# Optimization experiments

Hardware: AMD Instinct MI355X
Metric: run time of the kernel (lower is better)

Reference implementation:

```python
import jax, jax.numpy as jnp
import numpy as np

B, N, D = 2, 8192, 64          # batch, points, feature dim (dim_in == dim_out)
FILTER_SIZE = 11               # k nearest neighbors in feature space
N_ITER = 5                     # mean-field iterations


def setup_inputs() -> dict:
    key = jax.random.key(0)
    k0, k1, k2, k3 = jax.random.split(key, 4)
    return {
        "logits": jax.random.normal(k0, (B, N), jnp.float32),
        "p": jax.random.normal(k1, (B, D, N), jnp.float32),
        "W1": jax.random.normal(k2, (D, D), jnp.float32) / np.float32(np.sqrt(D)),
        "b1": jnp.zeros((D,), jnp.float32),
        "W2": jax.random.normal(k3, (D, D), jnp.float32) / np.float32(np.sqrt(D)),
        "b2": jnp.zeros((D,), jnp.float32),
    }


def reference(logits, p, W1, b1, W2, b2):
    # crf_encoder: two stacked Linear layers applied to p.permute(0,2,1) -> [B,N,D]
    f = jnp.einsum('bdn,de->bne', p, W1) + b1
    f = jnp.einsum('bne,ef->bnf', f, W2) + b2  # [B,N,D] feature embedding

    # pairwise squared distances in feature space: [B,N,N]
    sq = jnp.sum(f * f, axis=-1)
    d2 = sq[:, :, None] + sq[:, None, :] - 2.0 * jnp.einsum('bnd,bmd->bnm', f, f)

    # filter_size nearest neighbors (includes self) with Gaussian weights exp(-d2)
    neg_d2, idx = jax.lax.top_k(-d2, FILTER_SIZE)   # [B,N,K]
    w = jnp.exp(neg_d2)                             # [B,N,K]

    gather = jax.vmap(lambda qb, ib: qb[ib])        # per-batch gather: [N],[N,K]->[N,K]

    # mean-field iterations (binary CRF: sigmoid marginals, unary = logits)
    u = logits
    for _ in range(N_ITER):
        q = jax.nn.sigmoid(u)                       # current marginals [B,N]
        msg = jnp.sum(w * gather(q, idx), axis=-1)  # filtered message   [B,N]
        u = logits - msg                            # compatibility transform + unary

    return jax.nn.sigmoid(u)  # return_log_proba=False -> probabilities, [B,N]
```

## Files before the change

kernel.cpp:

```cpp
#include <hip/hip_runtime.h>

#define NPTS 8192
#define NTOT 16384
#define KNB 11
#define CAP 16
#define MARG 9.0f
#define MAXM 8192

typedef __attribute__((ext_vector_type(8))) short short8;
typedef __attribute__((ext_vector_type(4))) float f32x4;

__device__ __forceinline__ unsigned short f2bf(float x) {
  union { float f; unsigned u; } v; v.f = x;
  unsigned r = v.u + 0x7FFFu + ((v.u >> 16) & 1u);
  return (unsigned short)(r >> 16);
}

__device__ __forceinline__ float sigm(float x) { return 1.f / (1.f + expf(-x)); }

__global__ __launch_bounds__(256) void k1_encode(
    const float* __restrict__ p,
    const float* __restrict__ W1,
    const float* __restrict__ b1,
    const float* __restrict__ W2,
    const float* __restrict__ b2,
    float* __restrict__ f32f,
    unsigned short* __restrict__ fpre,
    float* __restrict__ sq,
    float* __restrict__ sq32,
    unsigned* __restrict__ cnt,
    int* __restrict__ lctr) {
  __shared__ float sp[64 * 64];
  __shared__ float st[64 * 65];
  __shared__ float sPart[4][64];
  int t = threadIdx.x, lane = t & 63;
  int w = __builtin_amdgcn_readfirstlane(t >> 6);
  int e0 = w * 16;
  int base = blockIdx.x * 64;
  int b = base >> 13, n0 = base & (NPTS - 1);
  const float* pb = p + (size_t)b * 64 * NPTS + n0;

  if (w == 0) cnt[base + lane] = 0u;
  if (base == 0 && t == 0) *lctr = 0;

  int row = t >> 4, chunk = t & 15;
#pragma unroll
  for (int k = 0; k < 4; ++k) {
    int r = k * 16 + row;
    uint4 v = *(const uint4*)(pb + (size_t)r * NPTS + chunk * 4);
    *(uint4*)(sp + r * 64 + chunk * 4) = v;
  }
  __syncthreads();

  float tt[16];
#pragma unroll
  for (int j = 0; j < 16; ++j) tt[j] = b1[e0 + j];
#pragma unroll 8
  for (int d = 0; d < 64; ++d) {
    float pd = sp[d * 64 + lane];
#pragma unroll
    for (int j = 0; j < 16; ++j)
      tt[j] = fmaf(pd, W1[d * 64 + e0 + j], tt[j]);
  }
#pragma unroll
  for (int j = 0; j < 16; ++j) st[lane * 65 + e0 + j] = tt[j];
  __syncthreads();

  float f[16];
#pragma unroll
  for (int j = 0; j < 16; ++j) f[j] = b2[e0 + j];
#pragma unroll 8
  for (int d = 0; d < 64; ++d) {
    float td = st[lane * 65 + d];
#pragma unroll
    for (int j = 0; j < 16; ++j)
      f[j] = fmaf(td, W2[d * 64 + e0 + j], f[j]);
  }

  float s = 0.f;
#pragma unroll
  for (int j = 0; j < 16; ++j) s = fmaf(f[j], f[j], s);
  sPart[w][lane] = s;
  __syncthreads();
  if (w == 0) {
    float s32 = sPart[0][lane] + sPart[1][lane];
    float s64 = s32 + (sPart[2][lane] + sPart[3][lane]);
    sq32[base + lane] = s32;
    sq[base + lane] = s64;
  }

  f32x4* o4 = (f32x4*)(f32f + (size_t)(base + lane) * 64 + e0);
#pragma unroll
  for (int jj = 0; jj < 4; ++jj) {
    f32x4 v; v[0] = f[4 * jj]; v[1] = f[4 * jj + 1]; v[2] = f[4 * jj + 2]; v[3] = f[4 * jj + 3];
    o4[jj] = v;
  }
  if (w < 2) {
    unsigned* ob = (unsigned*)(fpre + (size_t)(base + lane) * 32 + e0);
#pragma unroll
    for (int jj = 0; jj < 8; ++jj) {
      unsigned lo = f2bf(f[2 * jj]);
      unsigned hi = f2bf(f[2 * jj + 1]);
      ob[jj] = lo | (hi << 16);
    }
  }
}

__global__ __launch_bounds__(256) void k2_gram_select(
    const unsigned short* __restrict__ fpre,
    const float* __restrict__ sq32,
    unsigned* __restrict__ cnt,
    unsigned* __restrict__ cand,
    int* __restrict__ lctr,
    int* __restrict__ list) {
  __shared__ uint4 sB[1024];
  int bid = blockIdx.x;
  int b = (bid >= 528) ? 1 : 0;
  int rem = bid - b * 528;
  int band = (int)((sqrtf(8.f * (float)rem + 1.f) - 1.f) * 0.5f);
  if (((band + 1) * (band + 2)) / 2 <= rem) band++;
  else if ((band * (band + 1)) / 2 > rem) band--;
  int seg = rem - (band * (band + 1)) / 2;

  int t = threadIdx.x;
  int lane = t & 63;
  int arow = lane & 15;
  int q = lane >> 4;
  int wave = t >> 6;
  int rowbase = band * 256 + wave * 64;
  int cbase = seg * 256;
  const unsigned short* fb = fpre + (size_t)b * NPTS * 32;
  const float* s32b = sq32 + b * NPTS;

  const uint4* gsrc = (const uint4*)fb + (size_t)seg * 1024;
  uint4 v[4];
#pragma unroll
  for (int k = 0; k < 4; ++k) v[k] = gsrc[t + k * 256];

  short8 afrag[4];
#pragma unroll
  for (int tr = 0; tr < 4; ++tr)
    afrag[tr] = *(const short8*)(fb + (size_t)(rowbase + tr * 16 + arow) * 32 + q * 8);

  f32x4 srq[4], hh[4];
#pragma unroll
  for (int tr = 0; tr < 4; ++tr) {
    srq[tr] = *(const f32x4*)(s32b + rowbase + tr * 16 + (q << 2));
    hh[tr] = 0.5f * srq[tr];
  }
  float thrc[16];
#pragma unroll
  for (int cc = 0; cc < 4; ++cc)
#pragma unroll
    for (int tc = 0; tc < 4; ++tc)
      thrc[cc * 4 + tc] = 0.5f * s32b[cbase + cc * 64 + tc * 16 + arow] - 0.5f * MARG;

#pragma unroll
  for (int k = 0; k < 4; ++k) {
    int c = t + k * 256;
    int r = c >> 2, qq = c & 3;
    sB[r * 4 + (qq ^ (r & 3))] = v[k];
  }
  __syncthreads();

  f32x4 z4 = {0.f, 0.f, 0.f, 0.f};
  unsigned hitmask = 0u;
#pragma unroll
  for (int cc = 0; cc < 4; ++cc)
#pragma unroll
    for (int tc = 0; tc < 4; ++tc) {
      int e = cc * 4 + tc;
      int rl = cc * 64 + tc * 16 + arow;
      short8 bf = *(const short8*)&sB[rl * 4 + (q ^ (rl & 3))];
      f32x4 a0 = __builtin_amdgcn_mfma_f32_16x16x32_bf16(afrag[0], bf, z4, 0, 0, 0);
      f32x4 a1 = __builtin_amdgcn_mfma_f32_16x16x32_bf16(afrag[1], bf, z4, 0, 0, 0);
      f32x4 a2 = __builtin_amdgcn_mfma_f32_16x16x32_bf16(afrag[2], bf, z4, 0, 0, 0);
      f32x4 a3 = __builtin_amdgcn_mfma_f32_16x16x32_bf16(afrag[3], bf, z4, 0, 0, 0);
      float m0 = fmaxf(fmaxf(a0[0] - hh[0][0], a0[1] - hh[0][1]),
                       fmaxf(a0[2] - hh[0][2], a0[3] - hh[0][3]));
      float m1 = fmaxf(fmaxf(a1[0] - hh[1][0], a1[1] - hh[1][1]),
                       fmaxf(a1[2] - hh[1][2], a1[3] - hh[1][3]));
      float m2 = fmaxf(fmaxf(a2[0] - hh[2][0], a2[1] - hh[2][1]),
                       fmaxf(a2[2] - hh[2][2], a2[3] - hh[2][3]));
      float m3 = fmaxf(fmaxf(a3[0] - hh[3][0], a3[1] - hh[3][1]),
                       fmaxf(a3[2] - hh[3][2], a3[3] - hh[3][3]));
      float m = fmaxf(fmaxf(m0, m1), fmaxf(m2, m3));
      if (__ballot(m > thrc[e])) hitmask |= (1u << e);
    }

  if (hitmask) {
#pragma unroll 1
    for (int e = 0; e < 16; ++e) {
      if (!(hitmask & (1u << e))) continue;
      int cc = e >> 2, tc = e & 3;
      int rl = cc * 64 + tc * 16 + arow;
      short8 bf = *(const short8*)&sB[rl * 4 + (q ^ (rl & 3))];
      int colpt = cbase + cc * 64 + tc * 16 + arow;
      float scv = s32b[colpt];
      f32x4 acc[4];
#pragma unroll
      for (int tr = 0; tr < 4; ++tr)
        acc[tr] = __builtin_amdgcn_mfma_f32_16x16x32_bf16(afrag[tr], bf, z4, 0, 0, 0);
#pragma unroll
      for (int tr = 0; tr < 4; ++tr)
#pragma unroll
        for (int rg = 0; rg < 4; ++rg) {
          float d2 = srq[tr][rg] + scv - 2.f * acc[tr][rg];
          if (d2 < MARG) {
            int rowpt = rowbase + tr * 16 + (q << 2) + rg;
            int gr = b * NPTS + rowpt;
            union { float f; unsigned u; } cv; cv.f = d2 + 16.f;
            unsigned kb = cv.u & 0xFFFFE000u;
            unsigned slot = atomicAdd(&cnt[gr], 1u);
            if (slot < CAP) cand[gr * CAP + slot] = kb | (unsigned)colpt;
            if (slot == 1u) {
              int ls = atomicAdd(lctr, 1);
              if (ls < MAXM) list[ls] = gr;
            }
            if (band != seg) {
              int gc = b * NPTS + colpt;
              unsigned slot2 = atomicAdd(&cnt[gc], 1u);
              if (slot2 < CAP) cand[gc * CAP + slot2] = kb | (unsigned)rowpt;
              if (slot2 == 1u) {
                int ls2 = atomicAdd(lctr, 1);
                if (ls2 < MAXM) list[ls2] = gc;
              }
            }
          }
        }
    }
  }
}

__global__ __launch_bounds__(256) void k3_fused(
    const float* __restrict__ f32f, const float* __restrict__ sq,
    const unsigned* __restrict__ cnt, const unsigned* __restrict__ cand,
    float* __restrict__ Wbuf, int* __restrict__ IDXb,
    const float* __restrict__ logits, float* __restrict__ out) {
  int r = blockIdx.x * 256 + threadIdx.x;
  int b = r >> 13;
  unsigned count = cnt[r];
  if (count <= 1u) {
    float lg = logits[r];
    float u = lg;
#pragma unroll
    for (int it = 0; it < 5; ++it) u = lg - sigm(u);
    out[r] = sigm(u);
    return;
  }
  if (count > CAP) count = CAP;

  unsigned k[CAP];
#pragma unroll
  for (int j = 0; j < CAP; ++j)
    k[j] = (j < (int)count) ? cand[r * CAP + j] : 0xFFFFFFFFu;
#pragma unroll
  for (int a = 0; a < CAP - 1; ++a)
#pragma unroll
    for (int c = 0; c < CAP - 1; ++c) {
      unsigned lo = min(k[c], k[c + 1]);
      unsigned hi = max(k[c], k[c + 1]);
      k[c] = lo; k[c + 1] = hi;
    }

  float fr[64];
  const f32x4* fr4 = (const f32x4*)(f32f + (size_t)r * 64);
#pragma unroll
  for (int j = 0; j < 16; ++j) {
    f32x4 v = fr4[j];
    fr[4 * j] = v[0]; fr[4 * j + 1] = v[1]; fr[4 * j + 2] = v[2]; fr[4 * j + 3] = v[3];
  }
  float sqr = sq[r];
  int nsel = (int)count < KNB ? (int)count : KNB;
#pragma unroll
  for (int kk = 0; kk < KNB; ++kk) {
    float w = 0.f;
    int gi = r;
    if (kk < nsel) {
      int col = (int)(k[kk] & 8191u);
      gi = b * NPTS + col;
      const float* fm = f32f + (size_t)gi * 64;
      float dot = 0.f;
#pragma unroll
      for (int d = 0; d < 64; ++d) dot = fmaf(fr[d], fm[d], dot);
      float d2 = sqr + sq[gi] - 2.f * dot;
      w = expf(-d2);
    }
    Wbuf[(size_t)r * KNB + kk] = w;
    IDXb[(size_t)r * KNB + kk] = gi;
  }
}

__global__ __launch_bounds__(1024) void kt_iter(
    const int* __restrict__ lctr, const int* __restrict__ list,
    const float* __restrict__ Wbuf, const int* __restrict__ IDXb,
    const float* __restrict__ logits, float* __restrict__ out) {
  __shared__ float qs[NTOT];
  __shared__ int slist[MAXM];
  __shared__ float su[MAXM];
  int t = threadIdx.x;
  int nm = *lctr; if (nm > MAXM) nm = MAXM;

#pragma unroll 1
  for (int k = t; k < nm; k += 1024) {
    int r = list[k];
    slist[k] = r;
    qs[r] = sigm(logits[r]);
  }
  __syncthreads();

  for (int it = 0; it < 5; ++it) {
#pragma unroll 1
    for (int k = t; k < nm; k += 1024) {
      int r = slist[k];
      float msg = 0.f;
      const float* wp = Wbuf + (size_t)r * KNB;
      const int* ip = IDXb + (size_t)r * KNB;
#pragma unroll
      for (int kk = 0; kk < KNB; ++kk) msg = fmaf(wp[kk], qs[ip[kk]], msg);
      su[k] = logits[r] - msg;
    }
    __syncthreads();
#pragma unroll 1
    for (int k = t; k < nm; k += 1024) qs[slist[k]] = sigm(su[k]);
    __syncthreads();
  }
#pragma unroll 1
  for (int k = t; k < nm; k += 1024) out[slist[k]] = sigm(su[k]);
}

extern "C" void kernel_launch(void* const* d_in, const int* in_sizes, int n_in,
                              void* d_out, int out_size, void* d_ws, size_t ws_size,
                              hipStream_t stream) {
  const float* logits = (const float*)d_in[0];
  const float* p      = (const float*)d_in[1];
  const float* W1     = (const float*)d_in[2];
  const float* b1     = (const float*)d_in[3];
  const float* W2     = (const float*)d_in[4];
  const float* b2     = (const float*)d_in[5];
  float* out = (float*)d_out;

  char* ws = (char*)d_ws;
  float* f32f = (float*)ws;
  unsigned short* fpre = (unsigned short*)(f32f + (size_t)NTOT * 64);
  float* sq = (float*)(fpre + (size_t)NTOT * 32);
  float* sq32 = sq + NTOT;
  unsigned* cnt = (unsigned*)(sq32 + NTOT);
  unsigned* cand = cnt + NTOT;
  float* Wbuf = (float*)(cand + (size_t)NTOT * CAP);
  int* IDX = (int*)(Wbuf + (size_t)NTOT * KNB);
  int* lctr = IDX + (size_t)NTOT * KNB;
  int* list = lctr + 1;

  k1_encode<<<256, 256, 0, stream>>>(p, W1, b1, W2, b2, f32f, fpre, sq, sq32, cnt, lctr);
  k2_gram_select<<<1056, 256, 0, stream>>>(fpre, sq32, cnt, cand, lctr, list);
  k3_fused<<<64, 256, 0, stream>>>(f32f, sq, cnt, cand, Wbuf, IDX, logits, out);
  kt_iter<<<1, 1024, 0, stream>>>(lctr, list, Wbuf, IDX, logits, out);
}
```

Measured before the change: 111.8 us.

## Fold row norm into MFMA accumulator and fuse neighbor weighting with iteration kernel

In the gram/select kernel, the row half-norm is passed as the negated MFMA accumulator init, so the per-element subtraction in the screening loop goes away. The k3 and kt_iter kernels are merged into one 65-block launch. Blocks 0-63 handle isolated points, and the last block (256 threads) does sorting, distance/weight computation and all mean-field iterations for the listed points. This removes one launch, but the per-candidate weight work moves from 64 parallel blocks onto a single 256-thread block, which may serialize it.

```diff
diff --git a/kernel.cpp b/kernel.cpp
--- a/kernel.cpp
+++ b/kernel.cpp
@@ -142,11 +142,11 @@
   for (int tr = 0; tr < 4; ++tr)
     afrag[tr] = *(const short8*)(fb + (size_t)(rowbase + tr * 16 + arow) * 32 + q * 8);
 
-  f32x4 srq[4], hh[4];
+  f32x4 srq[4], nh[4];
 #pragma unroll
   for (int tr = 0; tr < 4; ++tr) {
     srq[tr] = *(const f32x4*)(s32b + rowbase + tr * 16 + (q << 2));
-    hh[tr] = 0.5f * srq[tr];
+    nh[tr] = -0.5f * srq[tr];
   }
   float thrc[16];
 #pragma unroll
@@ -163,7 +163,6 @@
   }
   __syncthreads();
 
-  f32x4 z4 = {0.f, 0.f, 0.f, 0.f};
   unsigned hitmask = 0u;
 #pragma unroll
   for (int cc = 0; cc < 4; ++cc)
@@ -172,18 +171,14 @@
       int e = cc * 4 + tc;
       int rl = cc * 64 + tc * 16 + arow;
       short8 bf = *(const short8*)&sB[rl * 4 + (q ^ (rl & 3))];
-      f32x4 a0 = __builtin_amdgcn_mfma_f32_16x16x32_bf16(afrag[0], bf, z4, 0, 0, 0);
-      f32x4 a1 = __builtin_amdgcn_mfma_f32_16x16x32_bf16(afrag[1], bf, z4, 0, 0, 0);
-      f32x4 a2 = __builtin_amdgcn_mfma_f32_16x16x32_bf16(afrag[2], bf, z4, 0, 0, 0);
-      f32x4 a3 = __builtin_amdgcn_mfma_f32_16x16x32_bf16(afrag[3], bf, z4, 0, 0, 0);
-      float m0 = fmaxf(fmaxf(a0[0] - hh[0][0], a0[1] - hh[0][1]),
-                       fmaxf(a0[2] - hh[0][2], a0[3] - hh[0][3]));
-      float m1 = fmaxf(fmaxf(a1[0] - hh[1][0], a1[1] - hh[1][1]),
-                       fmaxf(a1[2] - hh[1][2], a1[3] - hh[1][3]));
-      float m2 = fmaxf(fmaxf(a2[0] - hh[2][0], a2[1] - hh[2][1]),
-                       fmaxf(a2[2] - hh[2][2], a2[3] - hh[2][3]));
-      float m3 = fmaxf(fmaxf(a3[0] - hh[3][0], a3[1] - hh[3][1]),
-                       fmaxf(a3[2] - hh[3][2], a3[3] - hh[3][3]));
+      f32x4 a0 = __builtin_amdgcn_mfma_f32_16x16x32_bf16(afrag[0], bf, nh[0], 0, 0, 0);
+      f32x4 a1 = __builtin_amdgcn_mfma_f32_16x16x32_bf16(afrag[1], bf, nh[1], 0, 0, 0);
+      f32x4 a2 = __builtin_amdgcn_mfma_f32_16x16x32_bf16(afrag[2], bf, nh[2], 0, 0, 0);
+      f32x4 a3 = __builtin_amdgcn_mfma_f32_16x16x32_bf16(afrag[3], bf, nh[3], 0, 0, 0);
+      float m0 = fmaxf(fmaxf(a0[0], a0[1]), fmaxf(a0[2], a0[3]));
+      float m1 = fmaxf(fmaxf(a1[0], a1[1]), fmaxf(a1[2], a1[3]));
+      float m2 = fmaxf(fmaxf(a2[0], a2[1]), fmaxf(a2[2], a2[3]));
+      float m3 = fmaxf(fmaxf(a3[0], a3[1]), fmaxf(a3[2], a3[3]));
       float m = fmaxf(fmaxf(m0, m1), fmaxf(m2, m3));
       if (__ballot(m > thrc[e])) hitmask |= (1u << e);
     }
@@ -200,12 +195,12 @@
       f32x4 acc[4];
 #pragma unroll
       for (int tr = 0; tr < 4; ++tr)
-        acc[tr] = __builtin_amdgcn_mfma_f32_16x16x32_bf16(afrag[tr], bf, z4, 0, 0, 0);
+        acc[tr] = __builtin_amdgcn_mfma_f32_16x16x32_bf16(afrag[tr], bf, nh[tr], 0, 0, 0);
 #pragma unroll
       for (int tr = 0; tr < 4; ++tr)
 #pragma unroll
         for (int rg = 0; rg < 4; ++rg) {
-          float d2 = srq[tr][rg] + scv - 2.f * acc[tr][rg];
+          float d2 = scv - 2.f * acc[tr][rg];
           if (d2 < MARG) {
             int rowpt = rowbase + tr * 16 + (q << 2) + rg;
             int gr = b * NPTS + rowpt;
@@ -232,86 +227,93 @@
   }
 }
 
-__global__ __launch_bounds__(256) void k3_fused(
+__global__ __launch_bounds__(256) void k3_final(
     const float* __restrict__ f32f, const float* __restrict__ sq,
     const unsigned* __restrict__ cnt, const unsigned* __restrict__ cand,
+    const int* __restrict__ lctr, const int* __restrict__ list,
     float* __restrict__ Wbuf, int* __restrict__ IDXb,
-    const float* __restrict__ logits, float* __restrict__ out) {
-  int r = blockIdx.x * 256 + threadIdx.x;
-  int b = r >> 13;
-  unsigned count = cnt[r];
-  if (count <= 1u) {
-    float lg = logits[r];
-    float u = lg;
-#pragma unroll
-    for (int it = 0; it < 5; ++it) u = lg - sigm(u);
-    out[r] = sigm(u);
-    return;
-  }
-  if (count > CAP) count = CAP;
-
-  unsigned k[CAP];
-#pragma unroll
-  for (int j = 0; j < CAP; ++j)
-    k[j] = (j < (int)count) ? cand[r * CAP + j] : 0xFFFFFFFFu;
-#pragma unroll
-  for (int a = 0; a < CAP - 1; ++a)
-#pragma unroll
-    for (int c = 0; c < CAP - 1; ++c) {
-      unsigned lo = min(k[c], k[c + 1]);
-      unsigned hi = max(k[c], k[c + 1]);
-      k[c] = lo; k[c + 1] = hi;
-    }
-
-  float fr[64];
-  const f32x4* fr4 = (const f32x4*)(f32f + (size_t)r * 64);
-#pragma unroll
-  for (int j = 0; j < 16; ++j) {
-    f32x4 v = fr4[j];
-    fr[4 * j] = v[0]; fr[4 * j + 1] = v[1]; fr[4 * j + 2] = v[2]; fr[4 * j + 3] = v[3];
-  }
-  float sqr = sq[r];
-  int nsel = (int)count < KNB ? (int)count : KNB;
-#pragma unroll
-  for (int kk = 0; kk < KNB; ++kk) {
-    float w = 0.f;
-    int gi = r;
-    if (kk < nsel) {
-      int col = (int)(k[kk] & 8191u);
-      gi = b * NPTS + col;
-      const float* fm = f32f + (size_t)gi * 64;
-      float dot = 0.f;
-#pragma unroll
-      for (int d = 0; d < 64; ++d) dot = fmaf(fr[d], fm[d], dot);
-      float d2 = sqr + sq[gi] - 2.f * dot;
-      w = expf(-d2);
-    }
-    Wbuf[(size_t)r * KNB + kk] = w;
-    IDXb[(size_t)r * KNB + kk] = gi;
-  }
-}
-
-__global__ __launch_bounds__(1024) void kt_iter(
-    const int* __restrict__ lctr, const int* __restrict__ list,
-    const float* __restrict__ Wbuf, const int* __restrict__ IDXb,
     const float* __restrict__ logits, float* __restrict__ out) {
   __shared__ float qs[NTOT];
   __shared__ int slist[MAXM];
   __shared__ float su[MAXM];
   int t = threadIdx.x;
+  int bid = blockIdx.x;
+
+  if (bid < 64) {
+    int r = bid * 256 + t;
+    unsigned count = cnt[r];
+    if (count <= 1u) {
+      float lg = logits[r];
+      float u = lg;
+#pragma unroll
+      for (int it = 0; it < 5; ++it) u = lg - sigm(u);
+      out[r] = sigm(u);
+    }
+    return;
+  }
+
   int nm = *lctr; if (nm > MAXM) nm = MAXM;
 
 #pragma unroll 1
-  for (int k = t; k < nm; k += 1024) {
+  for (int k = t; k < nm; k += 256) {
     int r = list[k];
     slist[k] = r;
     qs[r] = sigm(logits[r]);
   }
   __syncthreads();
 
+#pragma unroll 1
+  for (int k = t; k < nm; k += 256) {
+    int r = slist[k];
+    int b = r >> 13;
+    unsigned count = cnt[r];
+    if (count > CAP) count = CAP;
+
+    unsigned kc[CAP];
+#pragma unroll
+    for (int j = 0; j < CAP; ++j)
+      kc[j] = (j < (int)count) ? cand[r * CAP + j] : 0xFFFFFFFFu;
+#pragma unroll
+    for (int a = 0; a < CAP - 1; ++a)
+#pragma unroll
+      for (int c = 0; c < CAP - 1; ++c) {
+        unsigned lo = min(kc[c], kc[c + 1]);
+        unsigned hi = max(kc[c], kc[c + 1]);
+        kc[c] = lo; kc[c + 1] = hi;
+      }
+
+    float fr[64];
+    const f32x4* fr4 = (const f32x4*)(f32f + (size_t)r * 64);
+#pragma unroll
+    for (int j = 0; j < 16; ++j) {
+      f32x4 v = fr4[j];
+      fr[4 * j] = v[0]; fr[4 * j + 1] = v[1]; fr[4 * j + 2] = v[2]; fr[4 * j + 3] = v[3];
+    }
+    float sqr = sq[r];
+    int nsel = (int)count < KNB ? (int)count : KNB;
+#pragma unroll
+    for (int kk = 0; kk < KNB; ++kk) {
+      float w = 0.f;
+      int gi = r;
+      if (kk < nsel) {
+        int col = (int)(kc[kk] & 8191u);
+        gi = b * NPTS + col;
+        const float* fm = f32f + (size_t)gi * 64;
+        float dot = 0.f;
+#pragma unroll
+        for (int d = 0; d < 64; ++d) dot = fmaf(fr[d], fm[d], dot);
+        float d2 = sqr + sq[gi] - 2.f * dot;
+        w = expf(-d2);
+      }
+      Wbuf[(size_t)r * KNB + kk] = w;
+      IDXb[(size_t)r * KNB + kk] = gi;
+    }
+  }
+  __syncthreads();
+
   for (int it = 0; it < 5; ++it) {
 #pragma unroll 1
-    for (int k = t; k < nm; k += 1024) {
+    for (int k = t; k < nm; k += 256) {
       int r = slist[k];
       float msg = 0.f;
       const float* wp = Wbuf + (size_t)r * KNB;
@@ -322,11 +324,11 @@
     }
     __syncthreads();
 #pragma unroll 1
-    for (int k = t; k < nm; k += 1024) qs[slist[k]] = sigm(su[k]);
+    for (int k = t; k < nm; k += 256) qs[slist[k]] = sigm(su[k]);
     __syncthreads();
   }
 #pragma unroll 1
-  for (int k = t; k < nm; k += 1024) out[slist[k]] = sigm(su[k]);
+  for (int k = t; k < nm; k += 256) out[slist[k]] = sigm(su[k]);
 }
 
 extern "C" void kernel_launch(void* const* d_in, const int* in_sizes, int n_in,
@@ -354,6 +356,5 @@
 
   k1_encode<<<256, 256, 0, stream>>>(p, W1, b1, W2, b2, f32f, fpre, sq, sq32, cnt, lctr);
   k2_gram_select<<<1056, 256, 0, stream>>>(fpre, sq32, cnt, cand, lctr, list);
-  k3_fused<<<64, 256, 0, stream>>>(f32f, sq, cnt, cand, Wbuf, IDX, logits, out);
-  kt_iter<<<1, 1024, 0, stream>>>(lctr, list, Wbuf, IDX, logits, out);
-}
+  k3_final<<<65, 256, 0, stream>>>(f32f, sq, cnt, cand, lctr, list, Wbuf, IDX, logits, out);
+}
```

Result: faster. 108.0 us (-3.5%).
